# Optimization experiments

Measured on AMD Instinct MI355X. Metric: run time of the kernel, lower is better.

Reference implementation:

```python
import jax, jax.numpy as jnp
import numpy as np

MEM_DIM = 128
ORDER = 256
THETA = 256.0
BATCH = 16
SEQ = 256
IN_DIM = 128


def _lmu_discrete_AB(order, theta):
    # Legendre delay network matrices (same construction as GenerateABMatrix)
    Q = np.arange(order, dtype=np.float64)
    R = (2.0 * Q + 1.0)[:, None]
    j, i = np.meshgrid(Q, Q)
    A = np.where(i < j, -1.0, (-1.0) ** (i - j + 1)) * R          # (O, O)
    B = ((-1.0) ** Q[:, None]) * R                                 # (O, 1)
    At = A.T / theta                                               # transposed system
    Bt = B.T / theta                                               # (1, O)
    # ZOH discretization on the transposed system: expm of padded block matrix
    em = np.concatenate([np.concatenate([At, Bt], axis=0),
                         np.zeros((order + 1, 1))], axis=1)        # (O+1, O+1)
    ms = jax.scipy.linalg.expm(jnp.asarray(em, jnp.float32))
    Ad = ms[:order, :order]                                        # (O, O)
    Bd = ms[order:, :order]                                        # (1, O)
    return Ad, Bd


def setup_inputs() -> dict:
    key = jax.random.key(0)
    kx, kw = jax.random.split(key)
    x = jax.random.normal(kx, (BATCH, SEQ, IN_DIM), dtype=jnp.float32)
    # glorot-uniform MemoryKernel (inputDim, MemoryDim)
    limit = np.sqrt(6.0 / (IN_DIM + MEM_DIM))
    memory_kernel = jax.random.uniform(kw, (IN_DIM, MEM_DIM), dtype=jnp.float32,
                                       minval=-limit, maxval=limit)
    A, B_mat = _lmu_discrete_AB(ORDER, THETA)
    return {"x": x, "memory_kernel": memory_kernel, "A": A, "B_mat": B_mat}


def reference(x, memory_kernel, A, B_mat):
    """LRMUCell (hiddenCell=None, no memory/hidden feedback) unrolled over SEQ.

    Per step: u_t = x_t @ K ; m_t = m_{t-1} @ Ad + u_t[:, :, None] * Bd
    Returns the final flattened memory state (batch, MemoryDim * Order).
    """
    Bsz, T, D = x.shape
    M = memory_kernel.shape[1]
    O = A.shape[0]
    # No feedback into u, so the input projection can be hoisted out of the scan.
    u_all = jnp.einsum('btd,dm->tbm', x, memory_kernel)  # (T, B, M)

    def step(m, u):
        # m: (B, M, O); u: (B, M)
        # (B,M,1) @ (1,O) is an outer product along the last axes
        m_new = jnp.matmul(m, A) + u[..., None] * B_mat
        return m_new, None

    m0 = jnp.zeros((Bsz, M, O), dtype=x.dtype)
    m_final, _ = jax.lax.scan(step, m0, u_all)
    return m_final.reshape(Bsz, M * O)
```

## Files before the change

kernel.cpp:

```cpp
#include <hip/hip_runtime.h>


#define SEQ_T 256
#define DIM 128
#define ORD 256
#define BMROWS 2048

#define OFF_U 0
#define OFF_P (OFF_U + SEQ_T * BMROWS)
#define APSTRIDE (ORD * ORD + 2048)
#define OFF_AP (OFF_P + ORD * ORD + 2048)
#define OFF_FLAGS (OFF_AP + 7 * APSTRIDE + 2048)

#define LD_A(p) \
  __hip_atomic_load((p), __ATOMIC_RELAXED, __HIP_MEMORY_SCOPE_AGENT)
#define ST_A(p, v) \
  __hip_atomic_store((p), (v), __ATOMIC_RELAXED, __HIP_MEMORY_SCOPE_AGENT)

__device__ __forceinline__ void gbar(unsigned* flags, unsigned* gen,
                                     unsigned target) {
  asm volatile("s_waitcnt vmcnt(0)" ::: "memory");
  __syncthreads();
  const int tid = threadIdx.x;
  if (blockIdx.x == 0) {
    if (tid == 0) ST_A(&flags[0], target);
    while (LD_A(&flags[tid]) < target) __builtin_amdgcn_s_sleep(1);
    __syncthreads();
    if (tid == 0) ST_A(gen, target);
  } else {
    if (tid == 0) {
      ST_A(&flags[blockIdx.x], target);
      while (LD_A(gen) < target) __builtin_amdgcn_s_sleep(1);
    }
  }
  __syncthreads();
}

__global__ __launch_bounds__(256) void lrmu_all(
    const float* __restrict__ x, const float* __restrict__ K,
    const float* __restrict__ A, const float* __restrict__ Bm,
    float* __restrict__ out, float* __restrict__ ws) {
  __shared__ __align__(16) float Slds[ORD * 64];
  __shared__ __align__(16) float lsb[2048];
  __shared__ __align__(16) float redb[4 * 320];
  float* U = ws + OFF_U;
  float* P = ws + OFF_P;
  unsigned* flags = (unsigned*)(ws + OFF_FLAGS);
  unsigned* gen = flags + 320;
  const int blk = blockIdx.x, tid = threadIdx.x;

  {
    int b = blk >> 4, tc = blk & 15;
    float* xs = Slds;
    for (int idx = tid; idx < 16 * DIM; idx += 256)
      xs[idx] = x[(b * SEQ_T + tc * 16) * DIM + idx];
    __syncthreads();
    int m = tid & 127, th = tid >> 7;
    float acc[8] = {};
#pragma unroll 8
    for (int d = 0; d < DIM; ++d) {
      float kv = K[d * DIM + m];
#pragma unroll
      for (int r = 0; r < 8; ++r)
        acc[r] = fmaf(xs[(th * 8 + r) * DIM + d], kv, acc[r]);
    }
#pragma unroll
    for (int r = 0; r < 8; ++r)
      ST_A(&U[(tc * 16 + th * 8 + r) * BMROWS + b * DIM + m], acc[r]);
    if (blk == 0) ST_A(&P[tid], Bm[tid]);
    __syncthreads();
  }

  const int rg = blk >> 2, cg = blk & 3;
  const int lane = tid & 63, q = tid >> 6;
  const int ir = lane >> 4, c4 = (lane & 15) * 4;
  for (int k = 0; k < 8; ++k) {
    const float* S = (k == 0) ? A : (ws + OFF_AP + (k - 1) * APSTRIDE);
    float* Snew = ws + OFF_AP + ((k < 7) ? k : 6) * APSTRIDE;
    const int half = 1 << k;
    const int nsq = (k < 7) ? 4 : 0;
    const int ndb = (k == 7) ? 2 : (rg < half ? 1 : 0);
    const int nrows = nsq + ndb;

#pragma unroll
    for (int s = 0; s < 5; ++s) {
      float v = 0.f;
      if (s < nsq) {
        v = S[(4 * rg + s) * ORD + tid];
      } else if (s - nsq < ndb) {
        int d = rg + 64 * (s - nsq);
        v = (k == 0) ? Bm[tid] : P[d * ORD + tid];
      }
      lsb[s * ORD + tid] = v;
    }
#pragma unroll
    for (int j = 0; j < 16; ++j) {
      int f = tid + 256 * j;
      int i = f >> 4, cc = (f & 15) * 4;
      *(float4*)&Slds[i * 64 + cc] =
          *(const float4*)&S[i * ORD + cg * 64 + cc];
    }
    __syncthreads();

    float acc[5][4] = {};
#pragma unroll 4
    for (int ii = 0; ii < 16; ++ii) {
      int i = q * 64 + 4 * ii + ir;
      float4 sv = *(const float4*)&Slds[i * 64 + c4];
#pragma unroll
      for (int s = 0; s < 5; ++s) {
        float lv = lsb[s * ORD + i];
        acc[s][0] = fmaf(lv, sv.x, acc[s][0]);
        acc[s][1] = fmaf(lv, sv.y, acc[s][1]);
        acc[s][2] = fmaf(lv, sv.z, acc[s][2]);
        acc[s][3] = fmaf(lv, sv.w, acc[s][3]);
      }
    }
#pragma unroll
    for (int s = 0; s < 5; ++s)
#pragma unroll
      for (int w = 0; w < 4; ++w) {
        acc[s][w] += __shfl_xor(acc[s][w], 16);
        acc[s][w] += __shfl_xor(acc[s][w], 32);
      }
    if (ir == 0) {
#pragma unroll
      for (int s = 0; s < 5; ++s)
        *(float4*)&redb[q * 320 + s * 64 + c4] =
            make_float4(acc[s][0], acc[s][1], acc[s][2], acc[s][3]);
    }
    __syncthreads();
    for (int o = tid; o < 320; o += 256) {
      int s = o >> 6, c = o & 63;
      if (s < nrows) {
        float sum = redb[o] + redb[320 + o] + redb[640 + o] + redb[960 + o];
        if (s < nsq) {
          ST_A(&Snew[(4 * rg + s) * ORD + cg * 64 + c], sum);
        } else {
          int d = rg + 64 * (s - nsq);
          ST_A(&P[(half + d) * ORD + cg * 64 + c], sum);
        }
      }
    }
    if (k < 7) gbar(flags, gen, (unsigned)(k + 1));
  }

  asm volatile("s_waitcnt vmcnt(0)" ::: "memory");
  __syncthreads();
  if (tid == 0) ST_A(&flags[blk], 8u);

  {
    float* us = lsb;
    float* redo = Slds;
    int bm0 = blk * 8;
    for (int idx = tid; idx < SEQ_T * 8; idx += 256) {
      int t = idx >> 3, r = idx & 7;
      us[idx] = U[t * BMROWS + bm0 + r];
    }
    __syncthreads();
    int c4o = lane * 4, qo = q;
    float ao[8][4] = {};
#pragma unroll 4
    for (int tt = 0; tt < 32; ++tt) {
      int t = 128 + qo * 32 + tt;
      float4 pv = *(const float4*)&P[(SEQ_T - 1 - t) * ORD + c4o];
      float4 u0 = *(const float4*)&us[t * 8];
      float4 u1 = *(const float4*)&us[t * 8 + 4];
      float uv[8] = {u0.x, u0.y, u0.z, u0.w, u1.x, u1.y, u1.z, u1.w};
      float pw[4] = {pv.x, pv.y, pv.z, pv.w};
#pragma unroll
      for (int r = 0; r < 8; ++r)
#pragma unroll
        for (int w = 0; w < 4; ++w)
          ao[r][w] = fmaf(uv[r], pw[w], ao[r][w]);
    }
    if (blk == 0) {
      while (LD_A(&flags[tid]) < 8u) __builtin_amdgcn_s_sleep(1);
      __syncthreads();
      if (tid == 0) ST_A(gen, 8u);
    } else {
      if (tid == 0)
        while (LD_A(gen) < 8u) __builtin_amdgcn_s_sleep(1);
    }
    __syncthreads();
#pragma unroll 4
    for (int tt = 0; tt < 32; ++tt) {
      int t = qo * 32 + tt;
      float4 pv = *(const float4*)&P[(SEQ_T - 1 - t) * ORD + c4o];
      float4 u0 = *(const float4*)&us[t * 8];
      float4 u1 = *(const float4*)&us[t * 8 + 4];
      float uv[8] = {u0.x, u0.y, u0.z, u0.w, u1.x, u1.y, u1.z, u1.w};
      float pw[4] = {pv.x, pv.y, pv.z, pv.w};
#pragma unroll
      for (int r = 0; r < 8; ++r)
#pragma unroll
        for (int w = 0; w < 4; ++w)
          ao[r][w] = fmaf(uv[r], pw[w], ao[r][w]);
    }
#pragma unroll
    for (int r = 0; r < 8; ++r)
      *(float4*)&redo[qo * 2048 + r * 256 + c4o] =
          make_float4(ao[r][0], ao[r][1], ao[r][2], ao[r][3]);
    __syncthreads();
#pragma unroll
    for (int j = 0; j < 8; ++j) {
      int o = tid + 256 * j;
      float s = redo[o] + redo[2048 + o] + redo[4096 + o] + redo[6144 + o];
      out[bm0 * ORD + o] = s;
    }
  }
}

extern "C" void kernel_launch(void* const* d_in, const int* in_sizes, int n_in,
                              void* d_out, int out_size, void* d_ws,
                              size_t ws_size, hipStream_t stream) {
  const float* x = (const float*)d_in[0];
  const float* K = (const float*)d_in[1];
  const float* A = (const float*)d_in[2];
  const float* Bm = (const float*)d_in[3];
  float* out = (float*)d_out;
  float* ws = (float*)d_ws;

  hipMemsetAsync(ws + OFF_FLAGS, 0, 2048, stream);
  lrmu_all<<<256, 256, 0, stream>>>(x, K, A, Bm, out, ws);
}
```

Baseline: 119.7 us.

## Split persistent kernel across 512 blocks with half-width tiles per block

Measured after the change: 122.9 us. 1.03x slower.

```diff
diff --git a/kernel.cpp b/kernel.cpp
--- a/kernel.cpp
+++ b/kernel.cpp
@@ -5,6 +5,7 @@
 #define DIM 128
 #define ORD 256
 #define BMROWS 2048
+#define NBLK 512
 
 #define OFF_U 0
 #define OFF_P (OFF_U + SEQ_T * BMROWS)
@@ -24,7 +25,8 @@
   const int tid = threadIdx.x;
   if (blockIdx.x == 0) {
     if (tid == 0) ST_A(&flags[0], target);
-    while (LD_A(&flags[tid]) < target) __builtin_amdgcn_s_sleep(1);
+    while (LD_A(&flags[tid]) < target || LD_A(&flags[tid + 256]) < target)
+      __builtin_amdgcn_s_sleep(1);
     __syncthreads();
     if (tid == 0) ST_A(gen, target);
   } else {
@@ -40,40 +42,42 @@
     const float* __restrict__ x, const float* __restrict__ K,
     const float* __restrict__ A, const float* __restrict__ Bm,
     float* __restrict__ out, float* __restrict__ ws) {
-  __shared__ __align__(16) float Slds[ORD * 64];
+  __shared__ __align__(16) float Slds[ORD * 32];
   __shared__ __align__(16) float lsb[2048];
-  __shared__ __align__(16) float redb[4 * 320];
+  __shared__ __align__(16) float redb[4 * 160];
   float* U = ws + OFF_U;
   float* P = ws + OFF_P;
   unsigned* flags = (unsigned*)(ws + OFF_FLAGS);
-  unsigned* gen = flags + 320;
+  unsigned* gen = flags + 520;
   const int blk = blockIdx.x, tid = threadIdx.x;
 
   {
-    int b = blk >> 4, tc = blk & 15;
+    int b = blk >> 5, tc = blk & 31;
     float* xs = Slds;
-    for (int idx = tid; idx < 16 * DIM; idx += 256)
-      xs[idx] = x[(b * SEQ_T + tc * 16) * DIM + idx];
+    for (int idx = tid; idx < 8 * DIM; idx += 256)
+      xs[idx] = x[(b * SEQ_T + tc * 8) * DIM + idx];
     __syncthreads();
     int m = tid & 127, th = tid >> 7;
-    float acc[8] = {};
+    float acc[4] = {};
 #pragma unroll 8
     for (int d = 0; d < DIM; ++d) {
       float kv = K[d * DIM + m];
 #pragma unroll
-      for (int r = 0; r < 8; ++r)
-        acc[r] = fmaf(xs[(th * 8 + r) * DIM + d], kv, acc[r]);
-    }
-#pragma unroll
-    for (int r = 0; r < 8; ++r)
-      ST_A(&U[(tc * 16 + th * 8 + r) * BMROWS + b * DIM + m], acc[r]);
+      for (int r = 0; r < 4; ++r)
+        acc[r] = fmaf(xs[(th * 4 + r) * DIM + d], kv, acc[r]);
+    }
+#pragma unroll
+    for (int r = 0; r < 4; ++r)
+      ST_A(&U[(tc * 8 + th * 4 + r) * BMROWS + b * DIM + m], acc[r]);
     if (blk == 0) ST_A(&P[tid], Bm[tid]);
     __syncthreads();
   }
 
-  const int rg = blk >> 2, cg = blk & 3;
+  const int rg = blk >> 3, cg = blk & 7;
   const int lane = tid & 63, q = tid >> 6;
-  const int ir = lane >> 4, c4 = (lane & 15) * 4;
+  const int cl = lane & 7;
+  const int pr = (lane >> 3) & 1;
+  const int ir = lane >> 4;
   for (int k = 0; k < 8; ++k) {
     const float* S = (k == 0) ? A : (ws + OFF_AP + (k - 1) * APSTRIDE);
     float* Snew = ws + OFF_AP + ((k < 7) ? k : 6) * APSTRIDE;
@@ -94,19 +98,19 @@
       lsb[s * ORD + tid] = v;
     }
 #pragma unroll
-    for (int j = 0; j < 16; ++j) {
+    for (int j = 0; j < 8; ++j) {
       int f = tid + 256 * j;
-      int i = f >> 4, cc = (f & 15) * 4;
-      *(float4*)&Slds[i * 64 + cc] =
-          *(const float4*)&S[i * ORD + cg * 64 + cc];
+      int i = f >> 3, cc = (f & 7) * 4;
+      *(float4*)&Slds[i * 32 + cc] =
+          *(const float4*)&S[i * ORD + cg * 32 + cc];
     }
     __syncthreads();
 
     float acc[5][4] = {};
 #pragma unroll 4
-    for (int ii = 0; ii < 16; ++ii) {
-      int i = q * 64 + 4 * ii + ir;
-      float4 sv = *(const float4*)&Slds[i * 64 + c4];
+    for (int ii = 0; ii < 8; ++ii) {
+      int i = q * 64 + ir * 16 + ii * 2 + pr;
+      float4 sv = *(const float4*)&Slds[i * 32 + 4 * cl];
 #pragma unroll
       for (int s = 0; s < 5; ++s) {
         float lv = lsb[s * ORD + i];
@@ -120,25 +124,27 @@
     for (int s = 0; s < 5; ++s)
 #pragma unroll
       for (int w = 0; w < 4; ++w) {
+        acc[s][w] += __shfl_xor(acc[s][w], 8);
         acc[s][w] += __shfl_xor(acc[s][w], 16);
         acc[s][w] += __shfl_xor(acc[s][w], 32);
       }
-    if (ir == 0) {
+    if (lane < 8) {
 #pragma unroll
       for (int s = 0; s < 5; ++s)
-        *(float4*)&redb[q * 320 + s * 64 + c4] =
+        *(float4*)&redb[q * 160 + s * 32 + 4 * cl] =
             make_float4(acc[s][0], acc[s][1], acc[s][2], acc[s][3]);
     }
     __syncthreads();
-    for (int o = tid; o < 320; o += 256) {
-      int s = o >> 6, c = o & 63;
+    if (tid < 160) {
+      int s = tid >> 5, c = tid & 31;
       if (s < nrows) {
-        float sum = redb[o] + redb[320 + o] + redb[640 + o] + redb[960 + o];
+        float sum = redb[tid] + redb[160 + tid] + redb[320 + tid] +
+                    redb[480 + tid];
         if (s < nsq) {
-          ST_A(&Snew[(4 * rg + s) * ORD + cg * 64 + c], sum);
+          ST_A(&Snew[(4 * rg + s) * ORD + cg * 32 + c], sum);
         } else {
           int d = rg + 64 * (s - nsq);
-          ST_A(&P[(half + d) * ORD + cg * 64 + c], sum);
+          ST_A(&P[(half + d) * ORD + cg * 32 + c], sum);
         }
       }
     }
@@ -152,30 +158,29 @@
   {
     float* us = lsb;
     float* redo = Slds;
-    int bm0 = blk * 8;
-    for (int idx = tid; idx < SEQ_T * 8; idx += 256) {
-      int t = idx >> 3, r = idx & 7;
+    int bm0 = blk * 4;
+    for (int idx = tid; idx < SEQ_T * 4; idx += 256) {
+      int t = idx >> 2, r = idx & 3;
       us[idx] = U[t * BMROWS + bm0 + r];
     }
     __syncthreads();
     int c4o = lane * 4, qo = q;
-    float ao[8][4] = {};
+    float ao[4][4] = {};
 #pragma unroll 4
     for (int tt = 0; tt < 32; ++tt) {
       int t = 128 + qo * 32 + tt;
       float4 pv = *(const float4*)&P[(SEQ_T - 1 - t) * ORD + c4o];
-      float4 u0 = *(const float4*)&us[t * 8];
-      float4 u1 = *(const float4*)&us[t * 8 + 4];
-      float uv[8] = {u0.x, u0.y, u0.z, u0.w, u1.x, u1.y, u1.z, u1.w};
+      float4 uv = *(const float4*)&us[t * 4];
+      float u[4] = {uv.x, uv.y, uv.z, uv.w};
       float pw[4] = {pv.x, pv.y, pv.z, pv.w};
 #pragma unroll
-      for (int r = 0; r < 8; ++r)
-#pragma unroll
-        for (int w = 0; w < 4; ++w)
-          ao[r][w] = fmaf(uv[r], pw[w], ao[r][w]);
+      for (int r = 0; r < 4; ++r)
+#pragma unroll
+        for (int w = 0; w < 4; ++w) ao[r][w] = fmaf(u[r], pw[w], ao[r][w]);
     }
     if (blk == 0) {
-      while (LD_A(&flags[tid]) < 8u) __builtin_amdgcn_s_sleep(1);
+      while (LD_A(&flags[tid]) < 8u || LD_A(&flags[tid + 256]) < 8u)
+        __builtin_amdgcn_s_sleep(1);
       __syncthreads();
       if (tid == 0) ST_A(gen, 8u);
     } else {
@@ -187,25 +192,23 @@
     for (int tt = 0; tt < 32; ++tt) {
       int t = qo * 32 + tt;
       float4 pv = *(const float4*)&P[(SEQ_T - 1 - t) * ORD + c4o];
-      float4 u0 = *(const float4*)&us[t * 8];
-      float4 u1 = *(const float4*)&us[t * 8 + 4];
-      float uv[8] = {u0.x, u0.y, u0.z, u0.w, u1.x, u1.y, u1.z, u1.w};
+      float4 uv = *(const float4*)&us[t * 4];
+      float u[4] = {uv.x, uv.y, uv.z, uv.w};
       float pw[4] = {pv.x, pv.y, pv.z, pv.w};
 #pragma unroll
-      for (int r = 0; r < 8; ++r)
-#pragma unroll
-        for (int w = 0; w < 4; ++w)
-          ao[r][w] = fmaf(uv[r], pw[w], ao[r][w]);
-    }
-#pragma unroll
-    for (int r = 0; r < 8; ++r)
-      *(float4*)&redo[qo * 2048 + r * 256 + c4o] =
+      for (int r = 0; r < 4; ++r)
+#pragma unroll
+        for (int w = 0; w < 4; ++w) ao[r][w] = fmaf(u[r], pw[w], ao[r][w]);
+    }
+#pragma unroll
+    for (int r = 0; r < 4; ++r)
+      *(float4*)&redo[qo * 1024 + r * 256 + c4o] =
           make_float4(ao[r][0], ao[r][1], ao[r][2], ao[r][3]);
     __syncthreads();
 #pragma unroll
-    for (int j = 0; j < 8; ++j) {
+    for (int j = 0; j < 4; ++j) {
       int o = tid + 256 * j;
-      float s = redo[o] + redo[2048 + o] + redo[4096 + o] + redo[6144 + o];
+      float s = redo[o] + redo[1024 + o] + redo[2048 + o] + redo[3072 + o];
       out[bm0 * ORD + o] = s;
     }
   }
@@ -221,6 +224,6 @@
   float* out = (float*)d_out;
   float* ws = (float*)d_ws;
 
-  hipMemsetAsync(ws + OFF_FLAGS, 0, 2048, stream);
-  lrmu_all<<<256, 256, 0, stream>>>(x, K, A, Bm, out, ws);
+  hipMemsetAsync(ws + OFF_FLAGS, 0, 4096, stream);
+  lrmu_all<<<NBLK, 256, 0, stream>>>(x, K, A, Bm, out, ws);
 }
```

## Use radix-4 power doubling to halve grid barriers in the Bd·A^t table

Applied to the files above, without the earlier changes.

Result: slower. 213.5 us (+78.3%).

```diff
diff --git a/kernel.cpp b/kernel.cpp
--- a/kernel.cpp
+++ b/kernel.cpp
@@ -40,9 +40,10 @@
     const float* __restrict__ x, const float* __restrict__ K,
     const float* __restrict__ A, const float* __restrict__ Bm,
     float* __restrict__ out, float* __restrict__ ws) {
-  __shared__ __align__(16) float Slds[ORD * 64];
-  __shared__ __align__(16) float lsb[2048];
-  __shared__ __align__(16) float redb[4 * 320];
+  __shared__ __align__(16) float Slds[8192];
+  __shared__ __align__(16) float us[2048];
+  __shared__ __align__(16) float xb0[1024];
+  __shared__ __align__(16) float xb1[1024];
   float* U = ws + OFF_U;
   float* P = ws + OFF_P;
   unsigned* flags = (unsigned*)(ws + OFF_FLAGS);
@@ -71,98 +72,83 @@
     __syncthreads();
   }
 
-  const int rg = blk >> 2, cg = blk & 3;
-  const int lane = tid & 63, q = tid >> 6;
-  const int ir = lane >> 4, c4 = (lane & 15) * 4;
-  for (int k = 0; k < 8; ++k) {
-    const float* S = (k == 0) ? A : (ws + OFF_AP + (k - 1) * APSTRIDE);
-    float* Snew = ws + OFF_AP + ((k < 7) ? k : 6) * APSTRIDE;
-    const int half = 1 << k;
-    const int nsq = (k < 7) ? 4 : 0;
-    const int ndb = (k == 7) ? 2 : (rg < half ? 1 : 0);
-    const int nrows = nsq + ndb;
-
-#pragma unroll
-    for (int s = 0; s < 5; ++s) {
-      float v = 0.f;
-      if (s < nsq) {
-        v = S[(4 * rg + s) * ORD + tid];
-      } else if (s - nsq < ndb) {
-        int d = rg + 64 * (s - nsq);
-        v = (k == 0) ? Bm[tid] : P[d * ORD + tid];
+  for (int k = 0; k < 4; ++k) {
+    const int stride = 1 << (2 * k);
+    const float* Smat = (k == 0) ? A : (ws + OFF_AP + (k - 1) * APSTRIDE);
+    float* Snew = ws + OFF_AP + k * APSTRIDE;
+    const bool sq = (k < 3) && (blk < 64);
+    const bool pr = (k < 3) ? (blk >= 64 && blk < 64 + stride) : (blk < 64);
+    const int j = (k < 3) ? (blk - 64) : blk;
+
+    if (sq || pr) {
+      float* xc = xb0;
+      float* xn = xb1;
+      if (sq) {
+        float4 v;
+        v.x = Smat[(4 * blk + 0) * ORD + tid];
+        v.y = Smat[(4 * blk + 1) * ORD + tid];
+        v.z = Smat[(4 * blk + 2) * ORD + tid];
+        v.w = Smat[(4 * blk + 3) * ORD + tid];
+        *(float4*)&xc[4 * tid] = v;
+      } else {
+        float s0 = (k == 0) ? Bm[tid] : P[j * ORD + tid];
+        *(float4*)&xc[4 * tid] = make_float4(s0, 0.f, 0.f, 0.f);
       }
-      lsb[s * ORD + tid] = v;
-    }
-#pragma unroll
-    for (int j = 0; j < 16; ++j) {
-      int f = tid + 256 * j;
-      int i = f >> 4, cc = (f & 15) * 4;
-      *(float4*)&Slds[i * 64 + cc] =
-          *(const float4*)&S[i * ORD + cg * 64 + cc];
-    }
-    __syncthreads();
-
-    float acc[5][4] = {};
+      __syncthreads();
+#pragma unroll
+      for (int st = 0; st < 3; ++st) {
+        float a0 = 0.f, a1 = 0.f, a2 = 0.f, a3 = 0.f;
+        const float* Sc = Smat + tid;
 #pragma unroll 4
-    for (int ii = 0; ii < 16; ++ii) {
-      int i = q * 64 + 4 * ii + ir;
-      float4 sv = *(const float4*)&Slds[i * 64 + c4];
-#pragma unroll
-      for (int s = 0; s < 5; ++s) {
-        float lv = lsb[s * ORD + i];
-        acc[s][0] = fmaf(lv, sv.x, acc[s][0]);
-        acc[s][1] = fmaf(lv, sv.y, acc[s][1]);
-        acc[s][2] = fmaf(lv, sv.z, acc[s][2]);
-        acc[s][3] = fmaf(lv, sv.w, acc[s][3]);
-      }
-    }
-#pragma unroll
-    for (int s = 0; s < 5; ++s)
-#pragma unroll
-      for (int w = 0; w < 4; ++w) {
-        acc[s][w] += __shfl_xor(acc[s][w], 16);
-        acc[s][w] += __shfl_xor(acc[s][w], 32);
-      }
-    if (ir == 0) {
-#pragma unroll
-      for (int s = 0; s < 5; ++s)
-        *(float4*)&redb[q * 320 + s * 64 + c4] =
-            make_float4(acc[s][0], acc[s][1], acc[s][2], acc[s][3]);
-    }
-    __syncthreads();
-    for (int o = tid; o < 320; o += 256) {
-      int s = o >> 6, c = o & 63;
-      if (s < nrows) {
-        float sum = redb[o] + redb[320 + o] + redb[640 + o] + redb[960 + o];
-        if (s < nsq) {
-          ST_A(&Snew[(4 * rg + s) * ORD + cg * 64 + c], sum);
-        } else {
-          int d = rg + 64 * (s - nsq);
-          ST_A(&P[(half + d) * ORD + cg * 64 + c], sum);
+        for (int i = 0; i < 256; ++i) {
+          float4 xv = *(const float4*)&xc[4 * i];
+          float sv = Sc[i * ORD];
+          a0 = fmaf(xv.x, sv, a0);
+          a1 = fmaf(xv.y, sv, a1);
+          a2 = fmaf(xv.z, sv, a2);
+          a3 = fmaf(xv.w, sv, a3);
+        }
+        if (pr)
+          ST_A(&P[(j + (st + 1) * stride) * ORD + tid], a0);
+        if (st < 2) {
+          *(float4*)&xn[4 * tid] = make_float4(a0, a1, a2, a3);
+          __syncthreads();
+          float* t2 = xc; xc = xn; xn = t2;
+        } else if (sq) {
+          ST_A(&Snew[(4 * blk + 0) * ORD + tid], a0);
+          ST_A(&Snew[(4 * blk + 1) * ORD + tid], a1);
+          ST_A(&Snew[(4 * blk + 2) * ORD + tid], a2);
+          ST_A(&Snew[(4 * blk + 3) * ORD + tid], a3);
         }
       }
     }
-    if (k < 7) gbar(flags, gen, (unsigned)(k + 1));
+
+    if (k < 3) {
+      gbar(flags, gen, (unsigned)(k + 1));
+      if (k == 0) {
+        int bm0 = blk * 8;
+        for (int idx = tid; idx < SEQ_T * 8; idx += 256) {
+          int t = idx >> 3, r = idx & 7;
+          us[idx] = U[t * BMROWS + bm0 + r];
+        }
+      }
+    }
   }
 
   asm volatile("s_waitcnt vmcnt(0)" ::: "memory");
   __syncthreads();
-  if (tid == 0) ST_A(&flags[blk], 8u);
+  if (tid == 0) ST_A(&flags[blk], 4u);
 
   {
-    float* us = lsb;
     float* redo = Slds;
     int bm0 = blk * 8;
-    for (int idx = tid; idx < SEQ_T * 8; idx += 256) {
-      int t = idx >> 3, r = idx & 7;
-      us[idx] = U[t * BMROWS + bm0 + r];
-    }
-    __syncthreads();
-    int c4o = lane * 4, qo = q;
+    __syncthreads();
+    const int lane = tid & 63, qo = tid >> 6;
+    int c4o = lane * 4;
     float ao[8][4] = {};
 #pragma unroll 4
-    for (int tt = 0; tt < 32; ++tt) {
-      int t = 128 + qo * 32 + tt;
+    for (int tt = 0; tt < 16; ++tt) {
+      int t = 192 + qo * 16 + tt;
       float4 pv = *(const float4*)&P[(SEQ_T - 1 - t) * ORD + c4o];
       float4 u0 = *(const float4*)&us[t * 8];
       float4 u1 = *(const float4*)&us[t * 8 + 4];
@@ -171,21 +157,20 @@
 #pragma unroll
       for (int r = 0; r < 8; ++r)
 #pragma unroll
-        for (int w = 0; w < 4; ++w)
-          ao[r][w] = fmaf(uv[r], pw[w], ao[r][w]);
+        for (int w = 0; w < 4; ++w) ao[r][w] = fmaf(uv[r], pw[w], ao[r][w]);
     }
     if (blk == 0) {
-      while (LD_A(&flags[tid]) < 8u) __builtin_amdgcn_s_sleep(1);
+      while (LD_A(&flags[tid]) < 4u) __builtin_amdgcn_s_sleep(1);
       __syncthreads();
-      if (tid == 0) ST_A(gen, 8u);
+      if (tid == 0) ST_A(gen, 4u);
     } else {
       if (tid == 0)
-        while (LD_A(gen) < 8u) __builtin_amdgcn_s_sleep(1);
+        while (LD_A(gen) < 4u) __builtin_amdgcn_s_sleep(1);
     }
     __syncthreads();
 #pragma unroll 4
-    for (int tt = 0; tt < 32; ++tt) {
-      int t = qo * 32 + tt;
+    for (int tt = 0; tt < 48; ++tt) {
+      int t = qo * 48 + tt;
       float4 pv = *(const float4*)&P[(SEQ_T - 1 - t) * ORD + c4o];
       float4 u0 = *(const float4*)&us[t * 8];
       float4 u1 = *(const float4*)&us[t * 8 + 4];
@@ -194,8 +179,7 @@
 #pragma unroll
       for (int r = 0; r < 8; ++r)
 #pragma unroll
-        for (int w = 0; w < 4; ++w)
-          ao[r][w] = fmaf(uv[r], pw[w], ao[r][w]);
+        for (int w = 0; w < 4; ++w) ao[r][w] = fmaf(uv[r], pw[w], ao[r][w]);
     }
 #pragma unroll
     for (int r = 0; r < 8; ++r)
@@ -203,8 +187,8 @@
           make_float4(ao[r][0], ao[r][1], ao[r][2], ao[r][3]);
     __syncthreads();
 #pragma unroll
-    for (int j = 0; j < 8; ++j) {
-      int o = tid + 256 * j;
+    for (int j2 = 0; j2 < 8; ++j2) {
+      int o = tid + 256 * j2;
       float s = redo[o] + redo[2048 + o] + redo[4096 + o] + redo[6144 + o];
       out[bm0 * ORD + o] = s;
     }
```

## Drop final doubling step; apply A^128 to first-half partial state instead

Applied to the files above, without the earlier changes.

Result: no change. 121.8 us (+1.7%).

```diff
diff --git a/kernel.cpp b/kernel.cpp
--- a/kernel.cpp
+++ b/kernel.cpp
@@ -43,6 +43,7 @@
   __shared__ __align__(16) float Slds[ORD * 64];
   __shared__ __align__(16) float lsb[2048];
   __shared__ __align__(16) float redb[4 * 320];
+  __shared__ __align__(16) float v2b[2048];
   float* U = ws + OFF_U;
   float* P = ws + OFF_P;
   unsigned* flags = (unsigned*)(ws + OFF_FLAGS);
@@ -74,22 +75,20 @@
   const int rg = blk >> 2, cg = blk & 3;
   const int lane = tid & 63, q = tid >> 6;
   const int ir = lane >> 4, c4 = (lane & 15) * 4;
-  for (int k = 0; k < 8; ++k) {
+  for (int k = 0; k < 7; ++k) {
     const float* S = (k == 0) ? A : (ws + OFF_AP + (k - 1) * APSTRIDE);
-    float* Snew = ws + OFF_AP + ((k < 7) ? k : 6) * APSTRIDE;
+    float* Snew = ws + OFF_AP + k * APSTRIDE;
     const int half = 1 << k;
-    const int nsq = (k < 7) ? 4 : 0;
-    const int ndb = (k == 7) ? 2 : (rg < half ? 1 : 0);
-    const int nrows = nsq + ndb;
+    const int ndb = (rg < half) ? 1 : 0;
+    const int nrows = 4 + ndb;
 
 #pragma unroll
     for (int s = 0; s < 5; ++s) {
       float v = 0.f;
-      if (s < nsq) {
+      if (s < 4) {
         v = S[(4 * rg + s) * ORD + tid];
-      } else if (s - nsq < ndb) {
-        int d = rg + 64 * (s - nsq);
-        v = (k == 0) ? Bm[tid] : P[d * ORD + tid];
+      } else if (ndb) {
+        v = (k == 0) ? Bm[tid] : P[rg * ORD + tid];
       }
       lsb[s * ORD + tid] = v;
     }
@@ -134,24 +133,25 @@
       int s = o >> 6, c = o & 63;
       if (s < nrows) {
         float sum = redb[o] + redb[320 + o] + redb[640 + o] + redb[960 + o];
-        if (s < nsq) {
+        if (s < 4) {
           ST_A(&Snew[(4 * rg + s) * ORD + cg * 64 + c], sum);
         } else {
-          int d = rg + 64 * (s - nsq);
-          ST_A(&P[(half + d) * ORD + cg * 64 + c], sum);
+          ST_A(&P[(half + rg) * ORD + cg * 64 + c], sum);
         }
       }
     }
-    if (k < 7) gbar(flags, gen, (unsigned)(k + 1));
+    if (k < 6) gbar(flags, gen, (unsigned)(k + 1));
   }
 
   asm volatile("s_waitcnt vmcnt(0)" ::: "memory");
   __syncthreads();
-  if (tid == 0) ST_A(&flags[blk], 8u);
+  if (tid == 0) ST_A(&flags[blk], 7u);
 
   {
     float* us = lsb;
     float* redo = Slds;
+    float* band = Slds + 8192;
+    const float* A128 = ws + OFF_AP + 6 * APSTRIDE;
     int bm0 = blk * 8;
     for (int idx = tid; idx < SEQ_T * 8; idx += 256) {
       int t = idx >> 3, r = idx & 7;
@@ -161,8 +161,8 @@
     int c4o = lane * 4, qo = q;
     float ao[8][4] = {};
 #pragma unroll 4
-    for (int tt = 0; tt < 32; ++tt) {
-      int t = 128 + qo * 32 + tt;
+    for (int tt = 0; tt < 16; ++tt) {
+      int t = 192 + qo * 16 + tt;
       float4 pv = *(const float4*)&P[(SEQ_T - 1 - t) * ORD + c4o];
       float4 u0 = *(const float4*)&us[t * 8];
       float4 u1 = *(const float4*)&us[t * 8 + 4];
@@ -175,17 +175,17 @@
           ao[r][w] = fmaf(uv[r], pw[w], ao[r][w]);
     }
     if (blk == 0) {
-      while (LD_A(&flags[tid]) < 8u) __builtin_amdgcn_s_sleep(1);
+      while (LD_A(&flags[tid]) < 7u) __builtin_amdgcn_s_sleep(1);
       __syncthreads();
-      if (tid == 0) ST_A(gen, 8u);
+      if (tid == 0) ST_A(gen, 7u);
     } else {
       if (tid == 0)
-        while (LD_A(gen) < 8u) __builtin_amdgcn_s_sleep(1);
-    }
-    __syncthreads();
-#pragma unroll 4
-    for (int tt = 0; tt < 32; ++tt) {
-      int t = qo * 32 + tt;
+        while (LD_A(gen) < 7u) __builtin_amdgcn_s_sleep(1);
+    }
+    __syncthreads();
+#pragma unroll 4
+    for (int tt = 0; tt < 16; ++tt) {
+      int t = 128 + qo * 16 + tt;
       float4 pv = *(const float4*)&P[(SEQ_T - 1 - t) * ORD + c4o];
       float4 u0 = *(const float4*)&us[t * 8];
       float4 u1 = *(const float4*)&us[t * 8 + 4];
@@ -196,6 +196,56 @@
 #pragma unroll
         for (int w = 0; w < 4; ++w)
           ao[r][w] = fmaf(uv[r], pw[w], ao[r][w]);
+    }
+    float vo[8][4] = {};
+#pragma unroll 4
+    for (int tt = 0; tt < 32; ++tt) {
+      int t = qo * 32 + tt;
+      float4 pv = *(const float4*)&P[(127 - t) * ORD + c4o];
+      float4 u0 = *(const float4*)&us[t * 8];
+      float4 u1 = *(const float4*)&us[t * 8 + 4];
+      float uv[8] = {u0.x, u0.y, u0.z, u0.w, u1.x, u1.y, u1.z, u1.w};
+      float pw[4] = {pv.x, pv.y, pv.z, pv.w};
+#pragma unroll
+      for (int r = 0; r < 8; ++r)
+#pragma unroll
+        for (int w = 0; w < 4; ++w)
+          vo[r][w] = fmaf(uv[r], pw[w], vo[r][w]);
+    }
+#pragma unroll
+    for (int r = 0; r < 8; ++r)
+      *(float4*)&redo[qo * 2048 + r * 256 + c4o] =
+          make_float4(vo[r][0], vo[r][1], vo[r][2], vo[r][3]);
+    __syncthreads();
+#pragma unroll
+    for (int j = 0; j < 8; ++j) {
+      int o = tid + 256 * j;
+      v2b[o] = redo[o] + redo[2048 + o] + redo[4096 + o] + redo[6144 + o];
+    }
+    __syncthreads();
+    for (int b = 0; b < 8; ++b) {
+#pragma unroll
+      for (int j = 0; j < 8; ++j) {
+        int f = tid + 256 * j;
+        int il = f >> 6, cc = (f & 63) * 4;
+        *(float4*)&band[il * 256 + cc] =
+            *(const float4*)&A128[(32 * b + il) * ORD + cc];
+      }
+      __syncthreads();
+#pragma unroll
+      for (int ii = 0; ii < 8; ++ii) {
+        int il = 8 * qo + ii;
+        float4 av = *(const float4*)&band[il * 256 + c4o];
+        float aw[4] = {av.x, av.y, av.z, av.w};
+#pragma unroll
+        for (int r = 0; r < 8; ++r) {
+          float lv = v2b[r * 256 + 32 * b + il];
+#pragma unroll
+          for (int w = 0; w < 4; ++w)
+            ao[r][w] = fmaf(lv, aw[w], ao[r][w]);
+        }
+      }
+      __syncthreads();
     }
 #pragma unroll
     for (int r = 0; r < 8; ++r)
```
